# Kernel tuning notes

Hardware: AMD Instinct MI355X
Metric: run time of the kernel (lower is better)

The kernel has to match this reference:

```python
import jax, jax.numpy as jnp
import numpy as np

B, K, P = 16, 64, 256
D_MODEL, EXPAND = 512, 2
D_INNER = D_MODEL * EXPAND  # 1024
D_CONV, D_FF, E_LAYERS = 4, 16, 4
DT_RANK = 32  # ceil(512/16)
RANK = 4


def rmsnorm(x, w, eps=1e-5):
    return x * jax.lax.rsqrt(jnp.mean(x * x, axis=-1, keepdims=True) + eps) * w


def selective_scan(u, delta, A, Bm, Cm, Dp):
    # u,delta: [b,l,d]; A: [d,n]; Bm,Cm: [b,l,n]; Dp: [d]
    dA = jnp.exp(jnp.einsum('bld,dn->bldn', delta, A))
    dBu = jnp.einsum('bld,bln,bld->bldn', delta, Bm, u)
    x0 = jnp.zeros((u.shape[0], u.shape[2], A.shape[1]), u.dtype)

    def step(x, t):
        dA_t, dBu_t, c_t = t
        x = dA_t * x + dBu_t
        return x, jnp.einsum('bdn,bn->bd', x, c_t)

    _, ys = jax.lax.scan(step, x0, (dA.swapaxes(0, 1), dBu.swapaxes(0, 1), Cm.swapaxes(0, 1)))
    return ys.swapaxes(0, 1) + u * Dp


def mamba_block(h, in_w, cw, cb, xp_w, dt_w, dt_b, A_log, Dp, out_w):
    b, l, _ = h.shape
    xr = h @ in_w.T  # [b,l,2*d_inner]
    x, res = xr[..., :D_INNER], xr[..., D_INNER:]
    # causal depthwise conv1d (torch pads d_conv-1 both sides then trims to l)
    xc = jax.lax.conv_general_dilated(
        x.swapaxes(1, 2), cw, (1,), [(D_CONV - 1, 0)],
        feature_group_count=D_INNER, dimension_numbers=('NCH', 'OIH', 'NCH'))
    x = jax.nn.silu((xc + cb[:, None]).swapaxes(1, 2))
    A = -jnp.exp(A_log)
    x_dbl = x @ xp_w.T
    delta = jax.nn.softplus(x_dbl[..., :DT_RANK] @ dt_w.T + dt_b)
    Bm = x_dbl[..., DT_RANK:DT_RANK + D_FF]
    Cm = x_dbl[..., DT_RANK + D_FF:]
    y = selective_scan(x, delta, A, Bm, Cm, Dp)
    y = y * jax.nn.silu(res)
    return y @ out_w.T


def setup_inputs() -> dict:
    key = jax.random.key(0)
    ks = iter(jax.random.split(key, 32))
    rn = lambda s, sc=0.02: jax.random.normal(next(ks), s, jnp.float32) * sc
    A_init = jnp.log(jnp.tile(jnp.arange(1, D_FF + 1, dtype=jnp.float32)[None, None, :],
                              (E_LAYERS, D_INNER, 1)))
    return {
        'inputs': jax.random.normal(next(ks), (B, K, P), jnp.float32),
        'sp_lin1_w': rn((D_MODEL, P)), 'sp_lin1_b': jnp.zeros((D_MODEL,)),
        'sp_lin2_w': rn((D_MODEL, D_MODEL)), 'sp_lin2_b': jnp.zeros((D_MODEL,)),
        'sp_gate_w': rn((D_MODEL, P)), 'sp_gate_b': jnp.zeros((D_MODEL,)),
        'sp_norm_w': jnp.ones((D_MODEL,)),
        'in_proj_w': rn((E_LAYERS, 2 * D_INNER, D_MODEL)),
        'conv_w': rn((E_LAYERS, D_INNER, 1, D_CONV)),
        'conv_b': jnp.zeros((E_LAYERS, D_INNER)),
        'x_proj_w': rn((E_LAYERS, DT_RANK + 2 * D_FF, D_INNER)),
        'dt_proj_w': rn((E_LAYERS, D_INNER, DT_RANK)),
        'dt_proj_b': jnp.zeros((E_LAYERS, D_INNER)),
        'A_log': A_init,
        'D': jnp.ones((E_LAYERS, D_INNER)),
        'out_proj_w': rn((E_LAYERS, D_MODEL, D_INNER)),
        'blk_norm_w': jnp.ones((E_LAYERS, D_MODEL)),
        'post_norm_w': jnp.ones((D_MODEL,)),
        'proj_w': rn((2 * P * RANK, D_MODEL)),
    }


def reference(inputs, sp_lin1_w, sp_lin1_b, sp_lin2_w, sp_lin2_b, sp_gate_w, sp_gate_b,
              sp_norm_w, in_proj_w, conv_w, conv_b, x_proj_w, dt_proj_w, dt_proj_b,
              A_log, D, out_proj_w, blk_norm_w, post_norm_w, proj_w):
    # SpatialEncoder, shared across lags (pure last-dim linears -> apply to [B,K,P])
    h = jax.nn.gelu(inputs @ sp_lin1_w.T + sp_lin1_b, approximate=False)
    h = h @ sp_lin2_w.T + sp_lin2_b
    g = jax.nn.sigmoid(inputs @ sp_gate_w.T + sp_gate_b)
    h = rmsnorm(h * g, sp_norm_w)  # [B,K,d_model]
    for l in range(E_LAYERS):
        h = mamba_block(rmsnorm(h, blk_norm_w[l]), in_proj_w[l], conv_w[l], conv_b[l],
                        x_proj_w[l], dt_proj_w[l], dt_proj_b[l], A_log[l], D[l],
                        out_proj_w[l]) + h
    h = rmsnorm(h, post_norm_w)
    out = h @ proj_w.T  # [B,K,2*P*RANK]
    U = out[..., :P * RANK].reshape(B, K, P, RANK)
    V = out[..., P * RANK:].reshape(B, K, P, RANK)
    coeffs = jnp.einsum('bkpr,bkqr->bkpq', U, V)
    preds = jnp.einsum('bkpq,bkq->bp', coeffs, inputs)
    return preds, coeffs
```

## Files before the change

kernel.cpp:

```cpp
#include <hip/hip_runtime.h>
#include <hip/hip_bf16.h>
#include <math.h>

namespace {

constexpr int SEQ    = 64;
constexpr int DINNER = 1024;
constexpr int WXPD_STRIDE = 1056 * 1024;

typedef __attribute__((ext_vector_type(8))) short short8;
typedef __attribute__((ext_vector_type(4))) float f32x4;
typedef __attribute__((address_space(3))) unsigned int lds_u32_t;
typedef __attribute__((address_space(1))) unsigned int glb_u32_t;

__device__ __forceinline__ float sigm(float x) { return 1.f / (1.f + __expf(-x)); }
__device__ __forceinline__ short f2b(float v) {
    __hip_bfloat16 h = __float2bfloat16(v);
    return *(short*)&h;
}
__device__ __forceinline__ float b2f(short s) {
    union { unsigned u; float f; } c; c.u = ((unsigned)(unsigned short)s) << 16; return c.f;
}
__device__ __forceinline__ float softp(float v) {
    return fmaxf(v, 0.f) + log1pf(__expf(-fabsf(v)));
}

__device__ __forceinline__ void gemm_core64(
    f32x4 (&acc)[2][2],
    const short* __restrict__ A, int lda,
    const short* __restrict__ W, int ldw,
    int Kd, short* As, short* Bs, int m0, int n0)
{
    constexpr int SZ = 64 * 64;
    const int tid = threadIdx.x, wave = tid >> 6, lane = tid & 63;
    const int wm = wave >> 1, wn = wave & 1;
    const int l15 = lane & 15, kg = lane >> 4;

    const int r0 = tid >> 3,        s0 = tid & 7;
    const int r1 = 32 + (tid >> 3), s1 = s0;
    const short* srcA0 = A + (size_t)(m0 + r0) * lda + ((s0 ^ (r0 & 7)) * 8);
    const short* srcA1 = A + (size_t)(m0 + r1) * lda + ((s1 ^ (r1 & 7)) * 8);
    const short* srcB0 = W + (size_t)(n0 + r0) * ldw + ((s0 ^ (r0 & 7)) * 8);
    const short* srcB1 = W + (size_t)(n0 + r1) * ldw + ((s1 ^ (r1 & 7)) * 8);
    const int ob0 = wave * 512;
    const int ob1 = 2048 + wave * 512;

    const int nt = Kd >> 6;
    __builtin_amdgcn_global_load_lds((const glb_u32_t*)srcA0, (lds_u32_t*)(As + ob0), 16, 0, 0);
    __builtin_amdgcn_global_load_lds((const glb_u32_t*)srcA1, (lds_u32_t*)(As + ob1), 16, 0, 0);
    __builtin_amdgcn_global_load_lds((const glb_u32_t*)srcB0, (lds_u32_t*)(Bs + ob0), 16, 0, 0);
    __builtin_amdgcn_global_load_lds((const glb_u32_t*)srcB1, (lds_u32_t*)(Bs + ob1), 16, 0, 0);

    for (int t = 0; t < nt; t++) {
        __syncthreads();
        if (t + 1 < nt) {
            const int k0 = (t + 1) * 64;
            const int s = ((t + 1) & 1) * SZ;
            __builtin_amdgcn_global_load_lds((const glb_u32_t*)(srcA0 + k0), (lds_u32_t*)(As + s + ob0), 16, 0, 0);
            __builtin_amdgcn_global_load_lds((const glb_u32_t*)(srcA1 + k0), (lds_u32_t*)(As + s + ob1), 16, 0, 0);
            __builtin_amdgcn_global_load_lds((const glb_u32_t*)(srcB0 + k0), (lds_u32_t*)(Bs + s + ob0), 16, 0, 0);
            __builtin_amdgcn_global_load_lds((const glb_u32_t*)(srcB1 + k0), (lds_u32_t*)(Bs + s + ob1), 16, 0, 0);
        }
        const short* Ab = As + (t & 1) * SZ;
        const short* Bb = Bs + (t & 1) * SZ;
        short8 af[2][2], bfr[2][2];
#pragma unroll
        for (int hk = 0; hk < 2; hk++) {
#pragma unroll
            for (int mi = 0; mi < 2; mi++) {
                const int row = wm * 32 + mi * 16 + l15;
                af[hk][mi] = *(const short8*)(Ab + row * 64 + (((hk * 4 + kg) ^ (row & 7)) * 8));
            }
#pragma unroll
            for (int ni = 0; ni < 2; ni++) {
                const int row = wn * 32 + ni * 16 + l15;
                bfr[hk][ni] = *(const short8*)(Bb + row * 64 + (((hk * 4 + kg) ^ (row & 7)) * 8));
            }
        }
#pragma unroll
        for (int hk = 0; hk < 2; hk++)
#pragma unroll
            for (int mi = 0; mi < 2; mi++)
#pragma unroll
                for (int ni = 0; ni < 2; ni++)
                    acc[mi][ni] = __builtin_amdgcn_mfma_f32_16x16x32_bf16(af[hk][mi], bfr[hk][ni], acc[mi][ni], 0, 0, 0);
    }
}

__global__ __launch_bounds__(256) void prep_k(
    const float* __restrict__ lin1_w, const float* __restrict__ gate_w,
    const float* __restrict__ lin2_w, const float* __restrict__ in_proj_w,
    const float* __restrict__ out_proj_w, const float* __restrict__ proj_w,
    const float* __restrict__ x_proj_w, const float* __restrict__ dt_proj_w,
    const float* __restrict__ inputs, const float* __restrict__ blk_norm_w,
    const float* __restrict__ post_norm_w, const float* __restrict__ sp_norm_w,
    short* __restrict__ wlin1gb, short* __restrict__ wlin2b, short* __restrict__ winpb,
    short* __restrict__ woutpb, short* __restrict__ wprojb, short* __restrict__ wxpdb,
    short* __restrict__ inputsb, float* __restrict__ preds, float* __restrict__ ss)
{
    const int blk = blockIdx.x, tid = threadIdx.x;
    if (blk < 512) {
        const int wave = tid >> 6, lane = tid & 63;
        const int nrow = blk * 8 + wave * 2;
        const int l = nrow >> 10, n = nrow & 1023;
        const float* dtw0 = dt_proj_w + (size_t)l * 32768 + n * 32;
        const float* dtw1 = dtw0 + 32;
        const float* xpw = x_proj_w + (size_t)l * 65536;
        float4 a0[4] = {}, a1[4] = {};
        for (int r = 0; r < 32; r++) {
            const float s0 = dtw0[r], s1 = dtw1[r];
#pragma unroll
            for (int rep = 0; rep < 4; rep++) {
                const float4 xv = *(const float4*)(xpw + r * 1024 + rep * 256 + lane * 4);
                a0[rep].x = fmaf(s0, xv.x, a0[rep].x); a0[rep].y = fmaf(s0, xv.y, a0[rep].y);
                a0[rep].z = fmaf(s0, xv.z, a0[rep].z); a0[rep].w = fmaf(s0, xv.w, a0[rep].w);
                a1[rep].x = fmaf(s1, xv.x, a1[rep].x); a1[rep].y = fmaf(s1, xv.y, a1[rep].y);
                a1[rep].z = fmaf(s1, xv.z, a1[rep].z); a1[rep].w = fmaf(s1, xv.w, a1[rep].w);
            }
        }
        short* dst0 = wxpdb + (size_t)l * WXPD_STRIDE + (size_t)(32 + n) * 1024;
        short* dst1 = dst0 + 1024;
#pragma unroll
        for (int rep = 0; rep < 4; rep++) {
            union { short sh[4]; uint2 u; } p0, p1;
            p0.sh[0] = f2b(a0[rep].x); p0.sh[1] = f2b(a0[rep].y);
            p0.sh[2] = f2b(a0[rep].z); p0.sh[3] = f2b(a0[rep].w);
            p1.sh[0] = f2b(a1[rep].x); p1.sh[1] = f2b(a1[rep].y);
            p1.sh[2] = f2b(a1[rep].z); p1.sh[3] = f2b(a1[rep].w);
            *(uint2*)(dst0 + rep * 256 + lane * 4) = p0.u;
            *(uint2*)(dst1 + rep * 256 + lane * 4) = p1.u;
        }
    } else if (blk < 544) {
#pragma unroll
        for (int rep = 0; rep < 4; rep++) {
            const int idx = (blk - 512) * 4096 + rep * 1024 + tid * 4;
            const int l = idx >> 15, off = idx & 32767;
            const float4 v = *(const float4*)(x_proj_w + (size_t)l * 65536 + 32768 + off);
            union { short sh[4]; uint2 u; } pk;
            pk.sh[0] = f2b(v.x); pk.sh[1] = f2b(v.y); pk.sh[2] = f2b(v.z); pk.sh[3] = f2b(v.w);
            *(uint2*)(wxpdb + (size_t)l * WXPD_STRIDE + off) = pk.u;
        }
    } else if (blk < 1504) {
        constexpr int pre[8] = {0, 128, 256, 512, 4608, 6656, 7680, 7936};
        for (int vb = blk - 544; vb < 7936; vb += 960) {
            int s = 0;
#pragma unroll
            for (int i = 1; i < 7; i++) s += (vb >= pre[i]);
            const int e = (vb - pre[s]) * 1024 + tid * 4;
            const float* src; short* dst;
            bool hasG = false; const float* gp = nullptr;
            bool hasSp = false;
            if      (s == 0) { src = lin1_w + e;     dst = wlin1gb + e; }
            else if (s == 1) { src = gate_w + e;     dst = wlin1gb + 131072 + e; }
            else if (s == 2) { src = lin2_w + e;     dst = wlin2b + e; }
            else if (s == 3) { src = in_proj_w + e;  dst = winpb + e;
                               hasG = true; gp = blk_norm_w + (e >> 20) * 512 + (e & 511);
                               hasSp = ((e >> 20) == 0); }
            else if (s == 4) { src = out_proj_w + e; dst = woutpb + e; }
            else if (s == 5) { src = proj_w + e;     dst = wprojb + e;
                               hasG = true; gp = post_norm_w + (e & 511); }
            else             { src = inputs + e;     dst = inputsb + e; }
            float4 v = *(const float4*)src;
            if (hasG) {
                const float4 gv = *(const float4*)gp;
                v.x *= gv.x; v.y *= gv.y; v.z *= gv.z; v.w *= gv.w;
            }
            if (hasSp) {
                const float4 sv = *(const float4*)(sp_norm_w + (e & 511));
                v.x *= sv.x; v.y *= sv.y; v.z *= sv.z; v.w *= sv.w;
            }
            union { short sh[4]; uint2 u; } pk;
            pk.sh[0] = f2b(v.x); pk.sh[1] = f2b(v.y); pk.sh[2] = f2b(v.z); pk.sh[3] = f2b(v.w);
            *(uint2*)dst = pk.u;
        }
    } else {
        const int i = (blk - 1504) * 256 + tid;
        if (i < 4096) preds[i] = 0.f;
        else ss[i - 4096] = 0.f;
    }
}

__global__ __launch_bounds__(256) void lin1gate_k(
    const short* __restrict__ A, const short* __restrict__ W,
    const float* __restrict__ b1, const float* __restrict__ b2,
    short* __restrict__ h1b, float* __restrict__ g)
{
    __shared__ short As[2 * 64 * 64];
    __shared__ short Bs[2 * 64 * 64];
    f32x4 acc[2][2] = {};
    const int m0 = blockIdx.y * 64, n0 = blockIdx.x * 64;
    gemm_core64(acc, A, 256, W, 256, 256, As, Bs, m0, n0);
    const int lane = threadIdx.x & 63, wave = threadIdx.x >> 6;
    const int wm = wave >> 1, wn = wave & 1, l15 = lane & 15, kg = lane >> 4;
#pragma unroll
    for (int ni = 0; ni < 2; ni++) {
        const int col = n0 + wn * 32 + ni * 16 + l15;
        const bool isG = col >= 512;
        const float b = isG ? b2[col - 512] : b1[col];
#pragma unroll
        for (int mi = 0; mi < 2; mi++)
#pragma unroll
            for (int j = 0; j < 4; j++) {
                const int row = m0 + wm * 32 + mi * 16 + kg * 4 + j;
                const float v = acc[mi][ni][j] + b;
                if (isG) g[(size_t)row * 512 + (col - 512)] = sigm(v);
                else     h1b[(size_t)row * 512 + col] = f2b(0.5f * v * (1.f + erff(v * 0.70710678f)));
            }
    }
}

__global__ __launch_bounds__(256) void lin2_k(
    const short* __restrict__ A, const short* __restrict__ W,
    const float* __restrict__ bias, const float* __restrict__ g,
    const float* __restrict__ gsp, float* __restrict__ x, short* __restrict__ xb,
    float* __restrict__ ssS1, float* __restrict__ ssS2)
{
    __shared__ short As[2 * 64 * 64];
    __shared__ short Bs[2 * 64 * 64];
    f32x4 acc[2][2] = {};
    const int m0 = blockIdx.y * 64, n0 = blockIdx.x * 64;
    gemm_core64(acc, A, 512, W, 512, 512, As, Bs, m0, n0);
    const int lane = threadIdx.x & 63, wave = threadIdx.x >> 6;
    const int wm = wave >> 1, wn = wave & 1, l15 = lane & 15, kg = lane >> 4;
    float vs1[2][4] = {}, vs2[2][4] = {};
#pragma unroll
    for (int ni = 0; ni < 2; ni++) {
        const int col = n0 + wn * 32 + ni * 16 + l15;
        const float b = bias[col];
        const float gc = gsp[col];
#pragma unroll
        for (int mi = 0; mi < 2; mi++)
#pragma unroll
            for (int j = 0; j < 4; j++) {
                const int row = m0 + wm * 32 + mi * 16 + kg * 4 + j;
                const float v = (acc[mi][ni][j] + b) * g[(size_t)row * 512 + col];
                x[(size_t)row * 512 + col] = v;
                xb[(size_t)row * 512 + col] = f2b(v);
                vs1[mi][j] = fmaf(v, v, vs1[mi][j]);
                const float w = v * gc;
                vs2[mi][j] = fmaf(w, w, vs2[mi][j]);
            }
    }
#pragma unroll
    for (int mi = 0; mi < 2; mi++)
#pragma unroll
        for (int j = 0; j < 4; j++) {
            float t1 = vs1[mi][j], t2 = vs2[mi][j];
            t1 += __shfl_xor(t1, 1, 64); t2 += __shfl_xor(t2, 1, 64);
            t1 += __shfl_xor(t1, 2, 64); t2 += __shfl_xor(t2, 2, 64);
            t1 += __shfl_xor(t1, 4, 64); t2 += __shfl_xor(t2, 4, 64);
            t1 += __shfl_xor(t1, 8, 64); t2 += __shfl_xor(t2, 8, 64);
            if (l15 == 0) {
                const int row = m0 + wm * 32 + mi * 16 + kg * 4 + j;
                atomicAdd(ssS1 + row, t1);
                atomicAdd(ssS2 + row, t2);
            }
        }
}

union ConvU {
    struct { short As[2 * 64 * 64]; short Bs[2 * 64 * 64]; } gm;
    float cbuf[67][68];
};

template <int COMB>
__global__ __launch_bounds__(256) void inprojconv_k(
    const short* __restrict__ A, const short* __restrict__ W,
    const float* __restrict__ ssA, const float* __restrict__ ssB,
    const float* __restrict__ cw, const float* __restrict__ cb,
    short* __restrict__ xcb, short* __restrict__ srb)
{
    __shared__ ConvU u;
    f32x4 acc[2][2] = {};
    const int m0 = blockIdx.y * 64, n0 = blockIdx.x * 64;
    gemm_core64(acc, A, 512, W, 512, 512, u.gm.As, u.gm.Bs, m0, n0);
    const int tid = threadIdx.x;
    const int lane = tid & 63, wave = tid >> 6;
    const int wm = wave >> 1, wn = wave & 1, l15 = lane & 15, kg = lane >> 4;

#pragma unroll
    for (int mi = 0; mi < 2; mi++)
#pragma unroll
        for (int j = 0; j < 4; j++) {
            const int row = m0 + wm * 32 + mi * 16 + kg * 4 + j;
            float r;
            if constexpr (COMB) {
                const float rx = rsqrtf(ssA[row] * (1.f / 512.f) + 1e-5f);
                r = rx * rsqrtf(rx * rx * ssB[row] * (1.f / 512.f) + 1e-5f);
            } else {
                r = rsqrtf(ssA[row] * (1.f / 512.f) + 1e-5f);
            }
#pragma unroll
            for (int ni = 0; ni < 2; ni++) acc[mi][ni][j] *= r;
        }

    if (n0 < 1024) {
        const int ccol = tid & 63;
        const int rg = tid >> 6;
        const int d = n0 + ccol;
        const float4 w4 = *(const float4*)(cw + d * 4);
        const float bia = cb[d];

        __syncthreads();
#pragma unroll
        for (int mi = 0; mi < 2; mi++)
#pragma unroll
            for (int ni = 0; ni < 2; ni++)
#pragma unroll
                for (int j = 0; j < 4; j++)
                    u.cbuf[3 + wm * 32 + mi * 16 + kg * 4 + j][wn * 32 + ni * 16 + l15] = acc[mi][ni][j];
        for (int i = tid; i < 3 * 68; i += 256) u.cbuf[i / 68][i % 68] = 0.f;
        __syncthreads();
#pragma unroll 4
        for (int k = 0; k < 16; k++) {
            const int row = rg + 4 * k;
            float v = bia + w4.x * u.cbuf[row][ccol] + w4.y * u.cbuf[row + 1][ccol]
                          + w4.z * u.cbuf[row + 2][ccol] + w4.w * u.cbuf[row + 3][ccol];
            v = v * sigm(v);
            xcb[(size_t)(m0 + row) * 1024 + d] = f2b(v);
        }
    } else {
#pragma unroll
        for (int ni = 0; ni < 2; ni++) {
            const int scol = n0 - 1024 + wn * 32 + ni * 16 + l15;
#pragma unroll
            for (int mi = 0; mi < 2; mi++)
#pragma unroll
                for (int j = 0; j < 4; j++) {
                    const int row = m0 + wm * 32 + mi * 16 + kg * 4 + j;
                    const float v = acc[mi][ni][j];
                    srb[(size_t)row * 1024 + scol] = f2b(v * sigm(v));
                }
        }
    }
}

union XsU {
    struct { short As[2 * 64 * 32]; short Wd[2 * 64 * 32]; short BC[2 * 32 * 32]; } gm;
    struct { float dlt[64][68]; float BC[64][32]; short ub[64][64]; float yt[64][68]; } sc;
};

__global__ __launch_bounds__(256) void xpdscan_k(
    const short* __restrict__ A , const short* __restrict__ W ,
    const float* __restrict__ dtb, const float* __restrict__ Alog,
    const float* __restrict__ Dp, const short* __restrict__ srb, short* __restrict__ yb)
{
    __shared__ XsU u;
    const int dg = blockIdx.x, b = blockIdx.y;
    const int m0 = b * 64;
    const int tid = threadIdx.x;
    const int lane = tid & 63, wave = tid >> 6;
    const int wm = wave >> 1, wn = wave & 1, l15 = lane & 15, kg = lane >> 4;

    constexpr int SZA = 64 * 32, SZBC = 32 * 32;
    const int p = wave * 64 + lane;
    const short* srcA  = A + (size_t)(m0 + (p >> 2)) * 1024 + (p & 3) * 8;
    const short* srcWd = W + (size_t)(32 + dg * 64 + (p >> 2)) * 1024 + (p & 3) * 8;
    const short* srcBC = W + (size_t)(p >> 2) * 1024 + (p & 3) * 8;
    const int ob = (wave * 64) * 8;

    f32x4 accd[2][2] = {};
    f32x4 accx[2] = {};

    __builtin_amdgcn_global_load_lds((const glb_u32_t*)srcA,  (lds_u32_t*)(u.gm.As + ob), 16, 0, 0);
    __builtin_amdgcn_global_load_lds((const glb_u32_t*)srcWd, (lds_u32_t*)(u.gm.Wd + ob), 16, 0, 0);
    if (wave < 2)
        __builtin_amdgcn_global_load_lds((const glb_u32_t*)srcBC, (lds_u32_t*)(u.gm.BC + ob), 16, 0, 0);

    for (int t = 0; t < 32; t++) {
        __syncthreads();
        if (t + 1 < 32) {
            const int k0 = (t + 1) * 32;
            const int sA = ((t + 1) & 1) * SZA, sBC = ((t + 1) & 1) * SZBC;
            __builtin_amdgcn_global_load_lds((const glb_u32_t*)(srcA + k0),  (lds_u32_t*)(u.gm.As + sA + ob), 16, 0, 0);
            __builtin_amdgcn_global_load_lds((const glb_u32_t*)(srcWd + k0), (lds_u32_t*)(u.gm.Wd + sA + ob), 16, 0, 0);
            if (wave < 2)
                __builtin_amdgcn_global_load_lds((const glb_u32_t*)(srcBC + k0), (lds_u32_t*)(u.gm.BC + sBC + ob), 16, 0, 0);
        }
        const short* Ab  = u.gm.As + (t & 1) * SZA;
        const short* Wdb = u.gm.Wd + (t & 1) * SZA;
        const short* BCb = u.gm.BC + (t & 1) * SZBC;
        short8 af[2], wf[2], bcf;
#pragma unroll
        for (int mi = 0; mi < 2; mi++)
            af[mi] = *(const short8*)(Ab + (wm * 32 + mi * 16 + l15) * 32 + kg * 8);
#pragma unroll
        for (int ni = 0; ni < 2; ni++)
            wf[ni] = *(const short8*)(Wdb + (wn * 32 + ni * 16 + l15) * 32 + kg * 8);
        bcf = *(const short8*)(BCb + (wn * 16 + l15) * 32 + kg * 8);
#pragma unroll
        for (int mi = 0; mi < 2; mi++) {
#pragma unroll
            for (int ni = 0; ni < 2; ni++)
                accd[mi][ni] = __builtin_amdgcn_mfma_f32_16x16x32_bf16(af[mi], wf[ni], accd[mi][ni], 0, 0, 0);
            accx[mi] = __builtin_amdgcn_mfma_f32_16x16x32_bf16(af[mi], bcf, accx[mi], 0, 0, 0);
        }
    }

    __syncthreads();
#pragma unroll
    for (int ni = 0; ni < 2; ni++) {
        const int dl = wn * 32 + ni * 16 + l15;
        const float bb = dtb[dg * 64 + dl];
#pragma unroll
        for (int mi = 0; mi < 2; mi++)
#pragma unroll
            for (int j = 0; j < 4; j++)
                u.sc.dlt[wm * 32 + mi * 16 + kg * 4 + j][dl] = softp(accd[mi][ni][j] + bb);
    }
    {
        const int c = wn * 16 + l15;
#pragma unroll
        for (int mi = 0; mi < 2; mi++)
#pragma unroll
            for (int j = 0; j < 4; j++)
                u.sc.BC[wm * 32 + mi * 16 + kg * 4 + j][c] = accx[mi][j];
    }
#pragma unroll
    for (int k = 0; k < 2; k++) {
        const int c = tid + k * 256;
        const int row = c >> 3, sl = c & 7;
        *(uint4*)&u.sc.ub[row][sl * 8] =
            *(const uint4*)(A + (size_t)(m0 + row) * 1024 + dg * 64 + sl * 8);
    }
    __syncthreads();

    {
        const int d_l = tid >> 2;
        const int ns = (tid & 3) << 2;
        const int d = dg * 64 + d_l;
        float a[4], s[4];
#pragma unroll
        for (int n = 0; n < 4; n++) {
            a[n] = -__expf(Alog[(size_t)d * 16 + ns + n]);
            s[n] = 0.f;
        }
        const float dv = Dp[d];
        for (int l = 0; l < SEQ; l++) {
            const float dlt = u.sc.dlt[l][d_l];
            const float uu = b2f(u.sc.ub[l][d_l]);
            const float dbu = dlt * uu;
            float part = 0.f;
#pragma unroll
            for (int n = 0; n < 4; n++) {
                s[n] = __expf(dlt * a[n]) * s[n] + dbu * u.sc.BC[l][ns + n];
                part = fmaf(s[n], u.sc.BC[l][16 + ns + n], part);
            }
            part += __shfl_xor(part, 1, 64);
            part += __shfl_xor(part, 2, 64);
            if ((tid & 3) == 0) u.sc.yt[l][d_l] = part + uu * dv;
        }
    }
    __syncthreads();
#pragma unroll
    for (int k = 0; k < 2; k++) {
        const int c = tid + k * 256;
        const int row = c >> 3, sl = c & 7;
        const short8 rv = *(const short8*)(srb + (size_t)(m0 + row) * 1024 + dg * 64 + sl * 8);
        short8 out;
#pragma unroll
        for (int j = 0; j < 8; j++)
            out[j] = f2b(u.sc.yt[row][sl * 8 + j] * b2f(rv[j]));
        *(short8*)(yb + (size_t)(m0 + row) * 1024 + dg * 64 + sl * 8) = out;
    }
}

template <int FIRST>
__global__ __launch_bounds__(256) void outproj_k(
    const short* __restrict__ A, const short* __restrict__ W,
    float* __restrict__ h, short* __restrict__ hb, float* __restrict__ ss_out,
    const float* __restrict__ xsrc, const float* __restrict__ gsp,
    const float* __restrict__ ssS1)
{
    __shared__ short As[2 * 32 * 32];
    __shared__ short Bs[2 * 64 * 32];
    constexpr int SZA = 32 * 32, SZB = 64 * 32;
    const int m0 = blockIdx.y * 32, n0 = blockIdx.x * 64;
    const int tid = threadIdx.x, wave = tid >> 6, lane = tid & 63;
    const int l15 = lane & 15, kg = lane >> 4;

    const int p = wave * 64 + lane;
    const short* srcA = A + (size_t)(m0 + (p >> 2)) * 1024 + (p & 3) * 8;
    const short* srcB = W + (size_t)(n0 + (p >> 2)) * 1024 + (p & 3) * 8;
    const int ob = (wave * 64) * 8;

    f32x4 acc[2] = {};
    if (wave < 2)
        __builtin_amdgcn_global_load_lds((const glb_u32_t*)srcA, (lds_u32_t*)(As + ob), 16, 0, 0);
    __builtin_amdgcn_global_load_lds((const glb_u32_t*)srcB, (lds_u32_t*)(Bs + ob), 16, 0, 0);

    for (int t = 0; t < 32; t++) {
        __syncthreads();
        if (t + 1 < 32) {
            const int k0 = (t + 1) * 32;
            const int sA = ((t + 1) & 1) * SZA, sB = ((t + 1) & 1) * SZB;
            if (wave < 2)
                __builtin_amdgcn_global_load_lds((const glb_u32_t*)(srcA + k0), (lds_u32_t*)(As + sA + ob), 16, 0, 0);
            __builtin_amdgcn_global_load_lds((const glb_u32_t*)(srcB + k0), (lds_u32_t*)(Bs + sB + ob), 16, 0, 0);
        }
        const short* Ab = As + (t & 1) * SZA;
        const short* Bb = Bs + (t & 1) * SZB;
        short8 af[2], bf;
#pragma unroll
        for (int mi = 0; mi < 2; mi++)
            af[mi] = *(const short8*)(Ab + (mi * 16 + l15) * 32 + kg * 8);
        bf = *(const short8*)(Bb + (wave * 16 + l15) * 32 + kg * 8);
#pragma unroll
        for (int mi = 0; mi < 2; mi++)
            acc[mi] = __builtin_amdgcn_mfma_f32_16x16x32_bf16(af[mi], bf, acc[mi], 0, 0, 0);
    }

    const int col = n0 + wave * 16 + l15;
    const float gc = FIRST ? gsp[col] : 0.f;
    float vsq[2][4] = {};
#pragma unroll
    for (int mi = 0; mi < 2; mi++)
#pragma unroll
        for (int j = 0; j < 4; j++) {
            const int row = m0 + mi * 16 + kg * 4 + j;
            float hold;
            if constexpr (FIRST) {
                const float rx = rsqrtf(ssS1[row] * (1.f / 512.f) + 1e-5f);
                hold = xsrc[(size_t)row * 512 + col] * rx * gc;
            } else {
                hold = h[(size_t)row * 512 + col];
            }
            const float v = acc[mi][j] + hold;
            h[(size_t)row * 512 + col] = v;
            hb[(size_t)row * 512 + col] = f2b(v);
            vsq[mi][j] = v * v;
        }
#pragma unroll
    for (int mi = 0; mi < 2; mi++)
#pragma unroll
        for (int j = 0; j < 4; j++) {
            float t = vsq[mi][j];
            t += __shfl_xor(t, 1, 64);
            t += __shfl_xor(t, 2, 64);
            t += __shfl_xor(t, 4, 64);
            t += __shfl_xor(t, 8, 64);
            if (l15 == 0) {
                const int row = m0 + mi * 16 + kg * 4 + j;
                atomicAdd(ss_out + row, t);
            }
        }
}

__global__ __launch_bounds__(256) void projf_k(
    const short* __restrict__ A, const short* __restrict__ W,
    const float* __restrict__ ss_in, float* __restrict__ xr)
{
    __shared__ short As[2 * 64 * 64];
    __shared__ short Bs[2 * 64 * 64];
    f32x4 acc[2][2] = {};
    const int m0 = blockIdx.y * 64, n0 = blockIdx.x * 64;
    gemm_core64(acc, A, 512, W, 512, 512, As, Bs, m0, n0);
    const int lane = threadIdx.x & 63, wave = threadIdx.x >> 6;
    const int wm = wave >> 1, wn = wave & 1, l15 = lane & 15, kg = lane >> 4;
#pragma unroll
    for (int mi = 0; mi < 2; mi++)
#pragma unroll
        for (int j = 0; j < 4; j++) {
            const int row = m0 + wm * 32 + mi * 16 + kg * 4 + j;
            const float r = rsqrtf(ss_in[row] * (1.f / 512.f) + 1e-5f);
#pragma unroll
            for (int ni = 0; ni < 2; ni++) {
                const int col = n0 + wn * 32 + ni * 16 + l15;
                xr[(size_t)row * 2048 + col] = acc[mi][ni][j] * r;
            }
        }
}

__global__ __launch_bounds__(256) void coeffs_k(
    const float* __restrict__ outp, const float* __restrict__ inp,
    float* __restrict__ coeffs, float* __restrict__ preds)
{
    const int m = blockIdx.x;
    const int b = m >> 6;
    const int tid = threadIdx.x, wave = tid >> 6, lane = tid & 63;
    __shared__ float4 Us[256], Vs[256];
    __shared__ float ins[256];
    __shared__ float4 tpart[4];
    Us[tid] = *(const float4*)(outp + (size_t)m * 2048 + tid * 4);
    Vs[tid] = *(const float4*)(outp + (size_t)m * 2048 + 1024 + tid * 4);
    ins[tid] = inp[(size_t)m * 256 + tid];
    __syncthreads();
    const float4 vq0 = Vs[lane * 4 + 0], vq1 = Vs[lane * 4 + 1];
    const float4 vq2 = Vs[lane * 4 + 2], vq3 = Vs[lane * 4 + 3];
    float* cbase = coeffs + (size_t)m * 65536 + lane * 4;
#pragma unroll 4
    for (int i = 0; i < 64; i++) {
        const int pp = (wave << 6) + i;
        const float4 up = Us[pp];
        float4 c;
        c.x = up.x * vq0.x + up.y * vq0.y + up.z * vq0.z + up.w * vq0.w;
        c.y = up.x * vq1.x + up.y * vq1.y + up.z * vq1.z + up.w * vq1.w;
        c.z = up.x * vq2.x + up.y * vq2.y + up.z * vq2.z + up.w * vq2.w;
        c.w = up.x * vq3.x + up.y * vq3.y + up.z * vq3.z + up.w * vq3.w;
        *(float4*)(cbase + (size_t)pp * 256) = c;
    }
    const float iv = ins[tid];
    const float4 vm = Vs[tid];
    float4 t = make_float4(vm.x * iv, vm.y * iv, vm.z * iv, vm.w * iv);
#pragma unroll
    for (int off = 32; off > 0; off >>= 1) {
        t.x += __shfl_xor(t.x, off, 64);
        t.y += __shfl_xor(t.y, off, 64);
        t.z += __shfl_xor(t.z, off, 64);
        t.w += __shfl_xor(t.w, off, 64);
    }
    if (lane == 0) tpart[wave] = t;
    __syncthreads();
    const float4 t0 = tpart[0], t1 = tpart[1], t2 = tpart[2], t3 = tpart[3];
    const float4 tt = make_float4(t0.x + t1.x + t2.x + t3.x, t0.y + t1.y + t2.y + t3.y,
                                  t0.z + t1.z + t2.z + t3.z, t0.w + t1.w + t2.w + t3.w);
    const float4 up = Us[tid];
    const float pv = up.x * tt.x + up.y * tt.y + up.z * tt.z + up.w * tt.w;
    atomicAdd(preds + (size_t)b * 256 + tid, pv);
}

}

extern "C" void kernel_launch(void* const* d_in, const int* in_sizes, int n_in,
                              void* d_out, int out_size, void* d_ws, size_t ws_size,
                              hipStream_t stream)
{
    const float* inputs     = (const float*)d_in[0];
    const float* lin1_w     = (const float*)d_in[1];
    const float* lin1_b     = (const float*)d_in[2];
    const float* lin2_w     = (const float*)d_in[3];
    const float* lin2_b     = (const float*)d_in[4];
    const float* gate_w     = (const float*)d_in[5];
    const float* gate_b     = (const float*)d_in[6];
    const float* sp_norm_w  = (const float*)d_in[7];
    const float* in_proj_w  = (const float*)d_in[8];
    const float* conv_w     = (const float*)d_in[9];
    const float* conv_b     = (const float*)d_in[10];
    const float* x_proj_w   = (const float*)d_in[11];
    const float* dt_proj_w  = (const float*)d_in[12];
    const float* dt_proj_b  = (const float*)d_in[13];
    const float* A_log      = (const float*)d_in[14];
    const float* Dvec       = (const float*)d_in[15];
    const float* out_proj_w = (const float*)d_in[16];
    const float* blk_norm_w = (const float*)d_in[17];
    const float* post_norm_w= (const float*)d_in[18];
    const float* proj_w     = (const float*)d_in[19];

    float* ws = (float*)d_ws;
    float* h     = ws;
    float* xr    = ws + 524288;
    float* x     = ws + 2621440;
    float* g     = ws + 3145728;
    float* ss    = ws + 3670016;
    short* bfb     = (short*)(ws + 3676160);
    short* inputsb = bfb;
    short* h1b     = bfb + 262144;
    short* hb      = bfb + 786432;
    short* xcb     = bfb + 1310720;
    short* yb      = bfb + 2359296;
    short* xb      = yb;
    short* srb     = bfb + 3407872;
    short* wlin1gb = bfb + 4456448;
    short* wlin2b  = bfb + 4718592;
    short* winpb   = bfb + 4980736;
    short* woutpb  = bfb + 9175040;
    short* wprojb  = bfb + 11272192;
    short* wxpdb   = bfb + 12320768;
    float* preds  = (float*)d_out;
    float* coeffs = (float*)d_out + 4096;

    const dim3 blk(256);

    prep_k<<<dim3(1544), blk, 0, stream>>>(
        lin1_w, gate_w, lin2_w, in_proj_w, out_proj_w, proj_w, x_proj_w, dt_proj_w,
        inputs, blk_norm_w, post_norm_w, sp_norm_w,
        wlin1gb, wlin2b, winpb, woutpb, wprojb, wxpdb, inputsb, preds, ss);

    lin1gate_k<<<dim3(16, 16), blk, 0, stream>>>(inputsb, wlin1gb, lin1_b, gate_b, h1b, g);
    lin2_k<<<dim3(8, 16), blk, 0, stream>>>(h1b, wlin2b, lin2_b, g, sp_norm_w,
                                            x, xb, ss, ss + 5120);

    for (int l = 0; l < 4; l++) {
        if (l == 0)
            inprojconv_k<1><<<dim3(32, 16), blk, 0, stream>>>(
                xb, winpb, ss, ss + 5120,
                conv_w, conv_b, xcb, srb);
        else
            inprojconv_k<0><<<dim3(32, 16), blk, 0, stream>>>(
                hb, winpb + (size_t)l * 1048576, ss + l * 1024, nullptr,
                conv_w + (size_t)l * 4096, conv_b + l * 1024, xcb, srb);
        xpdscan_k<<<dim3(16, 16), blk, 0, stream>>>(
            xcb, wxpdb + (size_t)l * WXPD_STRIDE, dt_proj_b + l * 1024,
            A_log + (size_t)l * 16384, Dvec + l * 1024, srb, yb);
        if (l == 0)
            outproj_k<1><<<dim3(8, 32), blk, 0, stream>>>(yb, woutpb,
                h, hb, ss + 1024, x, sp_norm_w, ss);
        else
            outproj_k<0><<<dim3(8, 32), blk, 0, stream>>>(yb, woutpb + (size_t)l * 524288,
                h, hb, ss + (l + 1) * 1024, nullptr, nullptr, nullptr);
    }

    projf_k<<<dim3(32, 16), blk, 0, stream>>>(hb, wprojb, ss + 4096, xr);
    coeffs_k<<<dim3(1024), blk, 0, stream>>>(xr, inputs, coeffs, preds);
}
```

Before: 375.2 us.

## Split weight prep and overlap bulk conversion with lin1/gate GEMM; widen outproj K-tile

The weight-conversion prep kernel is split. A small early kernel converts only what lin1/gate and lin2 need and zeroes the accumulators. The bulk in_proj/out_proj/proj/x_proj conversion is folded into extra blocks of the lin1gate GEMM launch, so it runs alongside that GEMM instead of serialising before it. The outproj GEMM also moves from a 32-wide to a 64-wide K tile with XOR-swizzled LDS, halving loop iterations and barriers. The fused launch has non-uniform blocks whose conversion work may delay the GEMM blocks, and the LDS footprint of outproj grows.

```diff
diff --git a/kernel.cpp b/kernel.cpp
--- a/kernel.cpp
+++ b/kernel.cpp
@@ -87,21 +87,70 @@
     }
 }
 
-__global__ __launch_bounds__(256) void prep_k(
+__global__ __launch_bounds__(256) void prep_early_k(
     const float* __restrict__ lin1_w, const float* __restrict__ gate_w,
-    const float* __restrict__ lin2_w, const float* __restrict__ in_proj_w,
-    const float* __restrict__ out_proj_w, const float* __restrict__ proj_w,
+    const float* __restrict__ lin2_w, const float* __restrict__ inputs,
+    short* __restrict__ wlin1gb, short* __restrict__ wlin2b, short* __restrict__ inputsb,
+    float* __restrict__ preds, float* __restrict__ ss)
+{
+    const int blk = blockIdx.x, tid = threadIdx.x;
+    if (blk < 768) {
+        const float* src; short* dst;
+        int e;
+        if (blk < 128)      { e = blk * 1024 + tid * 4;          src = lin1_w + e;  dst = wlin1gb + e; }
+        else if (blk < 256) { e = (blk - 128) * 1024 + tid * 4;  src = gate_w + e;  dst = wlin1gb + 131072 + e; }
+        else if (blk < 512) { e = (blk - 256) * 1024 + tid * 4;  src = lin2_w + e;  dst = wlin2b + e; }
+        else                { e = (blk - 512) * 1024 + tid * 4;  src = inputs + e;  dst = inputsb + e; }
+        const float4 v = *(const float4*)src;
+        union { short sh[4]; uint2 u; } pk;
+        pk.sh[0] = f2b(v.x); pk.sh[1] = f2b(v.y); pk.sh[2] = f2b(v.z); pk.sh[3] = f2b(v.w);
+        *(uint2*)dst = pk.u;
+    } else {
+        const int i = (blk - 768) * 256 + tid;
+        if (i < 4096) preds[i] = 0.f;
+        else if (i < 10240) ss[i - 4096] = 0.f;
+    }
+}
+
+__global__ __launch_bounds__(256) void lin1gate_k(
+    const short* __restrict__ A, const short* __restrict__ W,
+    const float* __restrict__ b1, const float* __restrict__ b2,
+    short* __restrict__ h1b, float* __restrict__ g,
     const float* __restrict__ x_proj_w, const float* __restrict__ dt_proj_w,
-    const float* __restrict__ inputs, const float* __restrict__ blk_norm_w,
+    const float* __restrict__ in_proj_w, const float* __restrict__ out_proj_w,
+    const float* __restrict__ proj_w, const float* __restrict__ blk_norm_w,
     const float* __restrict__ post_norm_w, const float* __restrict__ sp_norm_w,
-    short* __restrict__ wlin1gb, short* __restrict__ wlin2b, short* __restrict__ winpb,
-    short* __restrict__ woutpb, short* __restrict__ wprojb, short* __restrict__ wxpdb,
-    short* __restrict__ inputsb, float* __restrict__ preds, float* __restrict__ ss)
-{
+    short* __restrict__ winpb, short* __restrict__ woutpb,
+    short* __restrict__ wprojb, short* __restrict__ wxpdb)
+{
+    __shared__ short As[2 * 64 * 64];
+    __shared__ short Bs[2 * 64 * 64];
     const int blk = blockIdx.x, tid = threadIdx.x;
-    if (blk < 512) {
+
+    if (blk < 256) {
+        f32x4 acc[2][2] = {};
+        const int m0 = (blk >> 4) * 64, n0 = (blk & 15) * 64;
+        gemm_core64(acc, A, 256, W, 256, 256, As, Bs, m0, n0);
+        const int lane = tid & 63, wave = tid >> 6;
+        const int wm = wave >> 1, wn = wave & 1, l15 = lane & 15, kg = lane >> 4;
+#pragma unroll
+        for (int ni = 0; ni < 2; ni++) {
+            const int col = n0 + wn * 32 + ni * 16 + l15;
+            const bool isG = col >= 512;
+            const float b = isG ? b2[col - 512] : b1[col];
+#pragma unroll
+            for (int mi = 0; mi < 2; mi++)
+#pragma unroll
+                for (int j = 0; j < 4; j++) {
+                    const int row = m0 + wm * 32 + mi * 16 + kg * 4 + j;
+                    const float v = acc[mi][ni][j] + b;
+                    if (isG) g[(size_t)row * 512 + (col - 512)] = sigm(v);
+                    else     h1b[(size_t)row * 512 + col] = f2b(0.5f * v * (1.f + erff(v * 0.70710678f)));
+                }
+        }
+    } else if (blk < 768) {
         const int wave = tid >> 6, lane = tid & 63;
-        const int nrow = blk * 8 + wave * 2;
+        const int nrow = (blk - 256) * 8 + wave * 2;
         const int l = nrow >> 10, n = nrow & 1023;
         const float* dtw0 = dt_proj_w + (size_t)l * 32768 + n * 32;
         const float* dtw1 = dtw0 + 32;
@@ -130,36 +179,35 @@
             *(uint2*)(dst0 + rep * 256 + lane * 4) = p0.u;
             *(uint2*)(dst1 + rep * 256 + lane * 4) = p1.u;
         }
-    } else if (blk < 544) {
+    } else if (blk < 800) {
 #pragma unroll
         for (int rep = 0; rep < 4; rep++) {
-            const int idx = (blk - 512) * 4096 + rep * 1024 + tid * 4;
+            const int idx = (blk - 768) * 4096 + rep * 1024 + tid * 4;
             const int l = idx >> 15, off = idx & 32767;
             const float4 v = *(const float4*)(x_proj_w + (size_t)l * 65536 + 32768 + off);
             union { short sh[4]; uint2 u; } pk;
             pk.sh[0] = f2b(v.x); pk.sh[1] = f2b(v.y); pk.sh[2] = f2b(v.z); pk.sh[3] = f2b(v.w);
             *(uint2*)(wxpdb + (size_t)l * WXPD_STRIDE + off) = pk.u;
         }
-    } else if (blk < 1504) {
-        constexpr int pre[8] = {0, 128, 256, 512, 4608, 6656, 7680, 7936};
-        for (int vb = blk - 544; vb < 7936; vb += 960) {
-            int s = 0;
-#pragma unroll
-            for (int i = 1; i < 7; i++) s += (vb >= pre[i]);
-            const int e = (vb - pre[s]) * 1024 + tid * 4;
+    } else {
+        for (int c = blk - 800; c < 7168; c += 960) {
             const float* src; short* dst;
             bool hasG = false; const float* gp = nullptr;
             bool hasSp = false;
-            if      (s == 0) { src = lin1_w + e;     dst = wlin1gb + e; }
-            else if (s == 1) { src = gate_w + e;     dst = wlin1gb + 131072 + e; }
-            else if (s == 2) { src = lin2_w + e;     dst = wlin2b + e; }
-            else if (s == 3) { src = in_proj_w + e;  dst = winpb + e;
-                               hasG = true; gp = blk_norm_w + (e >> 20) * 512 + (e & 511);
-                               hasSp = ((e >> 20) == 0); }
-            else if (s == 4) { src = out_proj_w + e; dst = woutpb + e; }
-            else if (s == 5) { src = proj_w + e;     dst = wprojb + e;
-                               hasG = true; gp = post_norm_w + (e & 511); }
-            else             { src = inputs + e;     dst = inputsb + e; }
+            int e;
+            if (c < 4096) {
+                e = c * 1024 + tid * 4;
+                src = in_proj_w + e; dst = winpb + e;
+                hasG = true; gp = blk_norm_w + (e >> 20) * 512 + (e & 511);
+                hasSp = ((e >> 20) == 0);
+            } else if (c < 6144) {
+                e = (c - 4096) * 1024 + tid * 4;
+                src = out_proj_w + e; dst = woutpb + e;
+            } else {
+                e = (c - 6144) * 1024 + tid * 4;
+                src = proj_w + e; dst = wprojb + e;
+                hasG = true; gp = post_norm_w + (e & 511);
+            }
             float4 v = *(const float4*)src;
             if (hasG) {
                 const float4 gv = *(const float4*)gp;
@@ -173,39 +221,6 @@
             pk.sh[0] = f2b(v.x); pk.sh[1] = f2b(v.y); pk.sh[2] = f2b(v.z); pk.sh[3] = f2b(v.w);
             *(uint2*)dst = pk.u;
         }
-    } else {
-        const int i = (blk - 1504) * 256 + tid;
-        if (i < 4096) preds[i] = 0.f;
-        else ss[i - 4096] = 0.f;
-    }
-}
-
-__global__ __launch_bounds__(256) void lin1gate_k(
-    const short* __restrict__ A, const short* __restrict__ W,
-    const float* __restrict__ b1, const float* __restrict__ b2,
-    short* __restrict__ h1b, float* __restrict__ g)
-{
-    __shared__ short As[2 * 64 * 64];
-    __shared__ short Bs[2 * 64 * 64];
-    f32x4 acc[2][2] = {};
-    const int m0 = blockIdx.y * 64, n0 = blockIdx.x * 64;
-    gemm_core64(acc, A, 256, W, 256, 256, As, Bs, m0, n0);
-    const int lane = threadIdx.x & 63, wave = threadIdx.x >> 6;
-    const int wm = wave >> 1, wn = wave & 1, l15 = lane & 15, kg = lane >> 4;
-#pragma unroll
-    for (int ni = 0; ni < 2; ni++) {
-        const int col = n0 + wn * 32 + ni * 16 + l15;
-        const bool isG = col >= 512;
-        const float b = isG ? b2[col - 512] : b1[col];
-#pragma unroll
-        for (int mi = 0; mi < 2; mi++)
-#pragma unroll
-            for (int j = 0; j < 4; j++) {
-                const int row = m0 + wm * 32 + mi * 16 + kg * 4 + j;
-                const float v = acc[mi][ni][j] + b;
-                if (isG) g[(size_t)row * 512 + (col - 512)] = sigm(v);
-                else     h1b[(size_t)row * 512 + col] = f2b(0.5f * v * (1.f + erff(v * 0.70710678f)));
-            }
     }
 }
 
@@ -472,42 +487,53 @@
     const float* __restrict__ xsrc, const float* __restrict__ gsp,
     const float* __restrict__ ssS1)
 {
-    __shared__ short As[2 * 32 * 32];
-    __shared__ short Bs[2 * 64 * 32];
-    constexpr int SZA = 32 * 32, SZB = 64 * 32;
+    __shared__ short As[2 * 32 * 64];
+    __shared__ short Bs[2 * 64 * 64];
+    constexpr int SZA = 32 * 64, SZB = 64 * 64;
     const int m0 = blockIdx.y * 32, n0 = blockIdx.x * 64;
     const int tid = threadIdx.x, wave = tid >> 6, lane = tid & 63;
     const int l15 = lane & 15, kg = lane >> 4;
 
-    const int p = wave * 64 + lane;
-    const short* srcA = A + (size_t)(m0 + (p >> 2)) * 1024 + (p & 3) * 8;
-    const short* srcB = W + (size_t)(n0 + (p >> 2)) * 1024 + (p & 3) * 8;
-    const int ob = (wave * 64) * 8;
+    const int ra = tid >> 3, sa = tid & 7;
+    const short* srcA = A + (size_t)(m0 + ra) * 1024 + ((sa ^ (ra & 7)) * 8);
+    const int rb1 = 32 + (tid >> 3);
+    const short* srcB0 = W + (size_t)(n0 + ra) * 1024 + ((sa ^ (ra & 7)) * 8);
+    const short* srcB1 = W + (size_t)(n0 + rb1) * 1024 + ((sa ^ (rb1 & 7)) * 8);
+    const int obA = wave * 512;
+    const int obB0 = wave * 512, obB1 = 2048 + wave * 512;
 
     f32x4 acc[2] = {};
-    if (wave < 2)
-        __builtin_amdgcn_global_load_lds((const glb_u32_t*)srcA, (lds_u32_t*)(As + ob), 16, 0, 0);
-    __builtin_amdgcn_global_load_lds((const glb_u32_t*)srcB, (lds_u32_t*)(Bs + ob), 16, 0, 0);
-
-    for (int t = 0; t < 32; t++) {
+    __builtin_amdgcn_global_load_lds((const glb_u32_t*)srcA,  (lds_u32_t*)(As + obA), 16, 0, 0);
+    __builtin_amdgcn_global_load_lds((const glb_u32_t*)srcB0, (lds_u32_t*)(Bs + obB0), 16, 0, 0);
+    __builtin_amdgcn_global_load_lds((const glb_u32_t*)srcB1, (lds_u32_t*)(Bs + obB1), 16, 0, 0);
+
+    for (int t = 0; t < 16; t++) {
         __syncthreads();
-        if (t + 1 < 32) {
-            const int k0 = (t + 1) * 32;
+        if (t + 1 < 16) {
+            const int k0 = (t + 1) * 64;
             const int sA = ((t + 1) & 1) * SZA, sB = ((t + 1) & 1) * SZB;
-            if (wave < 2)
-                __builtin_amdgcn_global_load_lds((const glb_u32_t*)(srcA + k0), (lds_u32_t*)(As + sA + ob), 16, 0, 0);
-            __builtin_amdgcn_global_load_lds((const glb_u32_t*)(srcB + k0), (lds_u32_t*)(Bs + sB + ob), 16, 0, 0);
+            __builtin_amdgcn_global_load_lds((const glb_u32_t*)(srcA + k0),  (lds_u32_t*)(As + sA + obA), 16, 0, 0);
+            __builtin_amdgcn_global_load_lds((const glb_u32_t*)(srcB0 + k0), (lds_u32_t*)(Bs + sB + obB0), 16, 0, 0);
+            __builtin_amdgcn_global_load_lds((const glb_u32_t*)(srcB1 + k0), (lds_u32_t*)(Bs + sB + obB1), 16, 0, 0);
         }
         const short* Ab = As + (t & 1) * SZA;
         const short* Bb = Bs + (t & 1) * SZB;
-        short8 af[2], bf;
-#pragma unroll
-        for (int mi = 0; mi < 2; mi++)
-            af[mi] = *(const short8*)(Ab + (mi * 16 + l15) * 32 + kg * 8);
-        bf = *(const short8*)(Bb + (wave * 16 + l15) * 32 + kg * 8);
-#pragma unroll
-        for (int mi = 0; mi < 2; mi++)
-            acc[mi] = __builtin_amdgcn_mfma_f32_16x16x32_bf16(af[mi], bf, acc[mi], 0, 0, 0);
+        short8 af[2][2], bf[2];
+#pragma unroll
+        for (int hk = 0; hk < 2; hk++) {
+#pragma unroll
+            for (int mi = 0; mi < 2; mi++) {
+                const int row = mi * 16 + l15;
+                af[hk][mi] = *(const short8*)(Ab + row * 64 + (((hk * 4 + kg) ^ (row & 7)) * 8));
+            }
+            const int rowb = wave * 16 + l15;
+            bf[hk] = *(const short8*)(Bb + rowb * 64 + (((hk * 4 + kg) ^ (rowb & 7)) * 8));
+        }
+#pragma unroll
+        for (int hk = 0; hk < 2; hk++)
+#pragma unroll
+            for (int mi = 0; mi < 2; mi++)
+                acc[mi] = __builtin_amdgcn_mfma_f32_16x16x32_bf16(af[hk][mi], bf[hk], acc[mi], 0, 0, 0);
     }
 
     const int col = n0 + wave * 16 + l15;
@@ -671,12 +697,15 @@
 
     const dim3 blk(256);
 
-    prep_k<<<dim3(1544), blk, 0, stream>>>(
-        lin1_w, gate_w, lin2_w, in_proj_w, out_proj_w, proj_w, x_proj_w, dt_proj_w,
-        inputs, blk_norm_w, post_norm_w, sp_norm_w,
-        wlin1gb, wlin2b, winpb, woutpb, wprojb, wxpdb, inputsb, preds, ss);
-
-    lin1gate_k<<<dim3(16, 16), blk, 0, stream>>>(inputsb, wlin1gb, lin1_b, gate_b, h1b, g);
+    prep_early_k<<<dim3(808), blk, 0, stream>>>(
+        lin1_w, gate_w, lin2_w, inputs, wlin1gb, wlin2b, inputsb, preds, ss);
+
+    lin1gate_k<<<dim3(1760), blk, 0, stream>>>(
+        inputsb, wlin1gb, lin1_b, gate_b, h1b, g,
+        x_proj_w, dt_proj_w, in_proj_w, out_proj_w, proj_w,
+        blk_norm_w, post_norm_w, sp_norm_w,
+        winpb, woutpb, wprojb, wxpdb);
+
     lin2_k<<<dim3(8, 16), blk, 0, stream>>>(h1b, wlin2b, lin2_b, g, sp_norm_w,
                                             x, xb, ss, ss + 5120);
 
```

Result: faster. 359.0 us (-4.3%).
